# Performance work log

Measured on AMD Instinct MI355X. Metric: run time of the kernel, lower is better.

The kernel has to match this reference:

```python
import jax, jax.numpy as jnp
import numpy as np

NUM_HEADS = 16
LN_EPS = 1e-5


def pos_encoding(length, d):
    pos = jnp.arange(length, dtype=jnp.float32)[:, None]
    i = jnp.arange(d, dtype=jnp.float32)[None, :]
    angle = pos / jnp.power(10000.0, (2.0 * jnp.floor(i / 2.0)) / d)
    return jnp.where((jnp.arange(d) % 2) == 0, jnp.sin(angle), jnp.cos(angle))


def rel_shift(x):
    # x: (B, H, l, m) -> TXL shift trick
    b, h, l, m = x.shape
    x = jnp.concatenate([x, jnp.zeros((b, h, l, 1), x.dtype)], axis=-1)
    x = x.reshape(b, h, l * (m + 1))
    return x[:, :, l - 1:-1].reshape(b, h, l, m)


def layer_norm(x, g, b):
    mu = jnp.mean(x, axis=-1, keepdims=True)
    var = jnp.mean(jnp.square(x - mu), axis=-1, keepdims=True)
    return (x - mu) * jax.lax.rsqrt(var + LN_EPS) * g + b


def setup_inputs() -> dict:
    key = jax.random.key(0)
    B, S, M, D, L, V = 2, 1024, 1024, 1024, 4, 32000
    ks = jax.random.split(key, 32)
    s = 0.02
    d = {
        'inputs': jax.random.randint(ks[0], (B, S), 0, V, dtype=jnp.int32),
        'mems': jax.random.normal(ks[1], (L, B, M, D), jnp.float32),
        'emb': jax.random.normal(ks[2], (V, D), jnp.float32) * s,
        'Wq': jax.random.normal(ks[3], (L, D, D), jnp.float32) * s,
        'bq': jnp.zeros((L, D), jnp.float32),
        'Wke': jax.random.normal(ks[4], (L, D, D), jnp.float32) * s,
        'bke': jnp.zeros((L, D), jnp.float32),
        'Wkr': jax.random.normal(ks[5], (L, D, D), jnp.float32) * s,
        'bkr': jnp.zeros((L, D), jnp.float32),
        'Wv': jax.random.normal(ks[6], (L, D, D), jnp.float32) * s,
        'bv': jnp.zeros((L, D), jnp.float32),
        'Wo': jax.random.normal(ks[7], (L, D, D), jnp.float32) * s,
        'bo': jnp.zeros((L, D), jnp.float32),
        'ln1_g': jnp.ones((L, D), jnp.float32),
        'ln1_b': jnp.zeros((L, D), jnp.float32),
        'W1': jax.random.normal(ks[8], (L, D, D), jnp.float32) * s,
        'b1': jnp.zeros((L, D), jnp.float32),
        'W2': jax.random.normal(ks[9], (L, D, D), jnp.float32) * s,
        'b2': jnp.zeros((L, D), jnp.float32),
        'ln2_g': jnp.ones((L, D), jnp.float32),
        'ln2_b': jnp.zeros((L, D), jnp.float32),
        'Wh': jax.random.normal(ks[10], (D, D), jnp.float32) * s,
        'bh': jnp.zeros((D,), jnp.float32),
        'Wf': jax.random.normal(ks[11], (D, V), jnp.float32) * s,
        'bf': jnp.zeros((V,), jnp.float32),
        'next_mem_len': 1024,
    }
    return d


def reference(inputs, mems, emb, Wq, bq, Wke, bke, Wkr, bkr, Wv, bv, Wo, bo,
              ln1_g, ln1_b, W1, b1, W2, b2, ln2_g, ln2_b, Wh, bh, Wf, bf,
              next_mem_len):
    B, S = inputs.shape
    L, _, M, D = mems.shape
    T = M + S
    H = NUM_HEADS
    dh = D // H
    sqrt_dk = jnp.sqrt(jnp.float32(dh))

    rel_enc = pos_encoding(T, D)[::-1]  # (T, D), reversed
    # look-ahead mask: query i may attend key j iff j <= i + M
    mask = (jnp.arange(T)[None, :] > (jnp.arange(S)[:, None] + M)).astype(jnp.float32)
    mask = mask[None, None] * -1e9  # (1,1,S,T)

    x = emb[inputs] * jnp.sqrt(jnp.float32(D))  # (B,S,D)

    for l in range(L):
        x_tilde = jnp.concatenate([mems[l], x], axis=1)  # (B,T,D)
        q = (x @ Wq[l] + bq[l]).reshape(B, S, H, dh).transpose(0, 2, 1, 3)
        k = (x_tilde @ Wke[l] + bke[l]).reshape(B, T, H, dh).transpose(0, 2, 1, 3)
        v = (x_tilde @ Wv[l] + bv[l]).reshape(B, T, H, dh).transpose(0, 2, 1, 3)
        A = jnp.einsum('bhsd,bhtd->bhst', q, k)
        Qr = (rel_enc @ Wkr[l] + bkr[l]).reshape(T, H, dh).transpose(1, 0, 2)  # (H,T,dh)
        B_hat = jnp.einsum('bhsd,htd->bhst', q, Qr)
        score = (A + rel_shift(B_hat)) / sqrt_dk + mask
        attn = jax.nn.softmax(score, axis=-1)
        ctx = jnp.einsum('bhst,bhtd->bhsd', attn, v)
        ctx = ctx.transpose(0, 2, 1, 3).reshape(B, S, D)
        attn_out = ctx @ Wo[l] + bo[l]
        h1 = layer_norm(x + attn_out, ln1_g[l], ln1_b[l])
        ff = jax.nn.gelu(h1 @ W1[l] + b1[l], approximate=False) @ W2[l] + b2[l]
        x = layer_norm(h1 + ff, ln2_g[l], ln2_b[l])

    x = jax.nn.gelu(x @ Wh + bh, approximate=False)
    logits = x @ Wf + bf
    return logits
```

## Files before the change

### kernel.cpp

```cpp
#include <hip/hip_runtime.h>
#include <hip/hip_bf16.h>
#include <math.h>

typedef __attribute__((ext_vector_type(4))) float f32x4;
typedef __attribute__((ext_vector_type(8))) short s16x8;

#define BB 2
#define SS 1024
#define MEM 1024
#define DD 1024
#define LL 4
#define VV 32000
#define TT 2048
#define NH 16
#define DH 64

__device__ __forceinline__ short f2bf(float f) {
    unsigned u = __float_as_uint(f);
    u += 0x7fffu + ((u >> 16) & 1u);
    return (short)(u >> 16);
}

__device__ __forceinline__ float gelu_f(float x) {
    return 0.5f * x * (1.0f + erff(x * 0.70710678118654752f));
}

__device__ __forceinline__ void gll16(const short* g, short* l) {
    __builtin_amdgcn_global_load_lds(
        (__attribute__((address_space(1))) void*)(short*)g,
        (__attribute__((address_space(3))) void*)l, 16, 0, 0);
}

template<int N> __device__ __forceinline__ void vm_wait() {
    if constexpr (N == 0)      asm volatile("s_waitcnt vmcnt(0)" ::: "memory");
    else if constexpr (N == 2) asm volatile("s_waitcnt vmcnt(2)" ::: "memory");
    else if constexpr (N == 3) asm volatile("s_waitcnt vmcnt(3)" ::: "memory");
    else if constexpr (N == 4) asm volatile("s_waitcnt vmcnt(4)" ::: "memory");
    else if constexpr (N == 6) asm volatile("s_waitcnt vmcnt(6)" ::: "memory");
    else                       asm volatile("s_waitcnt vmcnt(8)" ::: "memory");
}

template<int WM, int WN>
__global__ __launch_bounds__(256) void gemm_bf16(
    const short* __restrict__ A, const short* __restrict__ Bt,
    const float* __restrict__ bias, const float* __restrict__ bias2,
    int nsplit, void* __restrict__ Cv, int N, int K, int nby, int act, int obf)
{
    constexpr int BM = WM * 32, BN = WN * 32;
    constexpr int NA = BM / 64, NB = BN / 64;
    constexpr int L  = NA + NB;
    constexpr int ASZ = BM * 32, BSZ = BN * 32;
    __shared__ short a_s[3 * ASZ];
    __shared__ short b_s[3 * BSZ];
    const int tid  = threadIdx.x;
    const int lane = tid & 63;
    const int wave = tid >> 6;
    const int wr = wave >> 1, wc = wave & 1;
    const int fr = lane & 15, fg = lane >> 4;

    const int nwg = gridDim.x;
    const int bid = blockIdx.x;
    const int swz = ((nwg & 7) == 0) ? ((bid & 7) * (nwg >> 3) + (bid >> 3)) : bid;
    const size_t m0 = (size_t)(swz % nby) * BM;
    const size_t n0 = (size_t)(swz / nby) * BN;

    const short* gA[NA]; short* lA[NA];
    const short* gB[NB]; short* lB[NB];
    #pragma unroll
    for (int i = 0; i < NA; ++i) {
        const int s   = i * 256 + tid;
        const int row = (s >> 6) * 16 + (s & 15);
        const int ks  = (s >> 4) & 3;
        gA[i] = A + (m0 + row) * (size_t)K + ks * 8;
        lA[i] = &a_s[s * 8];
    }
    #pragma unroll
    for (int i = 0; i < NB; ++i) {
        const int s   = i * 256 + tid;
        const int nn  = (s >> 6) * 16 + (s & 15);
        const int ks  = (s >> 4) & 3;
        gB[i] = Bt + (n0 + nn) * (size_t)K + ks * 8;
        lB[i] = &b_s[s * 8];
    }

    auto stage = [&](int t, int buf) {
        const int koff = t << 5;
        #pragma unroll
        for (int i = 0; i < NA; ++i) gll16(gA[i] + koff, lA[i] + buf * ASZ);
        #pragma unroll
        for (int i = 0; i < NB; ++i) gll16(gB[i] + koff, lB[i] + buf * BSZ);
    };

    f32x4 acc[WM][WN] = {};

    const int nt = K >> 5;
    stage(0, 0);
    stage(1, 1);

    int cur = 0;
    for (int t = 0; t < nt; ++t) {
        if (t + 1 < nt) vm_wait<L>();
        else            vm_wait<0>();
        __builtin_amdgcn_s_barrier();
        __builtin_amdgcn_sched_barrier(0);
        if (t + 2 < nt) stage(t + 2, cur == 0 ? 2 : cur - 1);

        const short* ab = &a_s[cur * ASZ];
        const short* bb = &b_s[cur * BSZ];
        s16x8 af[WM], bf[WN];
        #pragma unroll
        for (int mi = 0; mi < WM; ++mi)
            af[mi] = *(const s16x8*)&ab[((wr*WM + mi)*64 + fg*16 + fr) * 8];
        #pragma unroll
        for (int ni = 0; ni < WN; ++ni)
            bf[ni] = *(const s16x8*)&bb[((wc*WN + ni)*64 + fg*16 + fr) * 8];
        #pragma unroll
        for (int mi = 0; mi < WM; ++mi)
            #pragma unroll
            for (int ni = 0; ni < WN; ++ni)
                acc[mi][ni] = __builtin_amdgcn_mfma_f32_16x16x32_bf16(
                    af[mi], bf[ni], acc[mi][ni], 0, 0, 0);
        cur = (cur == 2) ? 0 : cur + 1;
    }

    float* Cf = (float*)Cv;
    short* Cb = (short*)Cv;
    #pragma unroll
    for (int mi = 0; mi < WM; ++mi) {
        #pragma unroll
        for (int ni = 0; ni < WN; ++ni) {
            const size_t r0 = m0 + wr*WM*16 + mi*16 + fg*4;
            const size_t c  = n0 + wc*WN*16 + ni*16 + fr;
            const float bb = (c < (size_t)nsplit) ? bias[c] : bias2[c - nsplit];
            #pragma unroll
            for (int rg = 0; rg < 4; ++rg) {
                float vv = acc[mi][ni][rg] + bb;
                if (act) vv = gelu_f(vv);
                if (obf) Cb[(r0 + rg)*(size_t)N + c] = f2bf(vv);
                else     Cf[(r0 + rg)*(size_t)N + c] = vv;
            }
        }
    }
}

__global__ __launch_bounds__(256) void transpose7_kernel(
    const float* w0, const float* w1, const float* w2, const float* w3,
    const float* w4, const float* w5, const float* w6, short* out)
{
    __shared__ float t[32][33];
    const int z = blockIdx.z;
    const float* W;
    switch (z) {
        case 0: W = w0; break; case 1: W = w1; break; case 2: W = w2; break;
        case 3: W = w3; break; case 4: W = w4; break; case 5: W = w5; break;
        default: W = w6; break;
    }
    short* O = out + (size_t)z * DD * DD;
    const int tid = threadIdx.x;
    const int k0 = blockIdx.y * 32, n0 = blockIdx.x * 32;
    const int r = tid >> 3, c4 = (tid & 7) * 4;
    float4 v = *(const float4*)&W[(size_t)(k0 + r) * DD + n0 + c4];
    t[r][c4+0] = v.x; t[r][c4+1] = v.y; t[r][c4+2] = v.z; t[r][c4+3] = v.w;
    __syncthreads();
    short4 o;
    o.x = f2bf(t[c4+0][r]); o.y = f2bf(t[c4+1][r]);
    o.z = f2bf(t[c4+2][r]); o.w = f2bf(t[c4+3][r]);
    *(short4*)&O[(size_t)(n0 + r) * DD + k0 + c4] = o;
}

__global__ __launch_bounds__(256) void transposeF_kernel(
    const float* __restrict__ W, short* __restrict__ O)
{
    __shared__ float t[32][33];
    const int tid = threadIdx.x;
    const int k0 = blockIdx.y * 32, n0 = blockIdx.x * 32;
    const int r = tid >> 3, c4 = (tid & 7) * 4;
    float4 v = *(const float4*)&W[(size_t)(k0 + r) * VV + n0 + c4];
    t[r][c4+0] = v.x; t[r][c4+1] = v.y; t[r][c4+2] = v.z; t[r][c4+3] = v.w;
    __syncthreads();
    short4 o;
    o.x = f2bf(t[c4+0][r]); o.y = f2bf(t[c4+1][r]);
    o.z = f2bf(t[c4+2][r]); o.w = f2bf(t[c4+3][r]);
    *(short4*)&O[(size_t)(n0 + r) * DD + k0 + c4] = o;
}

__global__ __launch_bounds__(256) void attn_kernel(
    const short* __restrict__ q, const short* __restrict__ k,
    const short* __restrict__ v, const short* __restrict__ Qr,
    short* __restrict__ ctx, int kstr, int qstr)
{
    __shared__ short k_s[64][72];
    __shared__ short vT_s[64][72];
    __shared__ short qr_s[128][72];
    __shared__ float a_t[64][67];
    __shared__ short p_s[64][72];

    const int tid  = threadIdx.x;
    const int id   = blockIdx.x;
    const int bh   = id & 31;
    const int qi   = ((id >> 5) + bh) & 15;
    const int q0   = qi * 64;
    const int b    = bh >> 4;
    const int h    = bh & 15;
    const int hoff = h * DH;

    const int lane = tid & 63;
    const int wave = tid >> 6;
    const int fr   = lane & 15;
    const int fg   = lane >> 4;
    const int tk = tid >> 2, ck = (tid & 3) * 16;
    const int rq = tid >> 1, dq = (tid & 1) * 32;
    const int sr  = tid >> 2;
    const int sc0 = (tid & 3) * 16;

    const short* qrow = q + ((size_t)(b * SS + q0 + 16 * wave + fr)) * DD + hoff;
    s16x8 aq0 = *(const s16x8*)(qrow + fg * 8);
    s16x8 aq1 = *(const s16x8*)(qrow + 32 + fg * 8);

    float m_r = -1e30f, l_r = 0.0f;

    const int t_end = q0 + 64 + MEM;
    const int u0b   = SS - 1 - q0 - 63;

    s16x8 kf0, kf1, vf0, vf1, rf0, rf1, rf2, rf3;
    auto loadT = [&](int t0) {
        const short* kp = k + ((size_t)(b * TT + t0 + tk)) * kstr + hoff + ck;
        const short* vp = v + ((size_t)(b * TT + t0 + tk)) * kstr + hoff + ck;
        kf0 = *(const s16x8*)kp;  kf1 = *(const s16x8*)(kp + 8);
        vf0 = *(const s16x8*)vp;  vf1 = *(const s16x8*)(vp + 8);
        int u = t0 + u0b + rq;
        u = u < 0 ? 0 : (u > TT - 1 ? TT - 1 : u);
        const short* rp = Qr + (size_t)u * qstr + hoff + dq;
        rf0 = *(const s16x8*)rp;        rf1 = *(const s16x8*)(rp + 8);
        rf2 = *(const s16x8*)(rp + 16); rf3 = *(const s16x8*)(rp + 24);
    };
    loadT(0);

    f32x4 opv[4] = {};
    const int nlo = 3 - wave, nhi = 7 - wave;

    for (int t0 = 0; t0 < t_end; t0 += 64) {
        asm volatile("" ::: "memory");
        __builtin_amdgcn_s_barrier();
        __builtin_amdgcn_sched_barrier(0);
        {
            *(s16x8*)&k_s[tk][ck]     = kf0;
            *(s16x8*)&k_s[tk][ck + 8] = kf1;
            #pragma unroll
            for (int i = 0; i < 8; ++i) {
                const int d0 = ck + i, d1 = ck + 8 + i;
                vT_s[d0][tk ^ (((d0 >> 3) & 3) << 3)] = vf0[i];
                vT_s[d1][tk ^ (((d1 >> 3) & 3) << 3)] = vf1[i];
            }
            *(s16x8*)&qr_s[rq][dq]      = rf0;
            *(s16x8*)&qr_s[rq][dq + 8]  = rf1;
            *(s16x8*)&qr_s[rq][dq + 16] = rf2;
            *(s16x8*)&qr_s[rq][dq + 24] = rf3;
        }
        if (t0 + 64 < t_end) loadT(t0 + 64);
        asm volatile("s_waitcnt lgkmcnt(0)" ::: "memory");
        __builtin_amdgcn_s_barrier();
        __builtin_amdgcn_sched_barrier(0);

        {
            #pragma unroll
            for (int n = 0; n < 4; ++n) {
                s16x8 b0 = *(const s16x8*)&k_s[16*n + fr][fg * 8];
                s16x8 b1 = *(const s16x8*)&k_s[16*n + fr][32 + fg * 8];
                f32x4 ca = {0, 0, 0, 0};
                ca = __builtin_amdgcn_mfma_f32_16x16x32_bf16(aq0, b0, ca, 0, 0, 0);
                ca = __builtin_amdgcn_mfma_f32_16x16x32_bf16(aq1, b1, ca, 0, 0, 0);
                #pragma unroll
                for (int rg = 0; rg < 4; ++rg)
                    a_t[16*wave + 4*fg + rg][16*n + fr] = ca[rg];
            }
        }
        {
            #pragma unroll
            for (int n = 0; n < 8; ++n) {
                if (n < nlo || n > nhi) continue;
                s16x8 c0 = *(const s16x8*)&qr_s[16*n + fr][fg * 8];
                s16x8 c1 = *(const s16x8*)&qr_s[16*n + fr][32 + fg * 8];
                f32x4 cb = {0, 0, 0, 0};
                cb = __builtin_amdgcn_mfma_f32_16x16x32_bf16(aq0, c0, cb, 0, 0, 0);
                cb = __builtin_amdgcn_mfma_f32_16x16x32_bf16(aq1, c1, cb, 0, 0, 0);
                #pragma unroll
                for (int rg = 0; rg < 4; ++rg) {
                    const int r  = 16*wave + 4*fg + rg;
                    const int tl = 16*n + fr - 63 + r;
                    if ((unsigned)tl < 64u) a_t[r][tl] += cb[rg];
                }
            }
        }

        {
            const int sg = q0 + sr;
            float e[16];
            float mx = -1e30f;
            #pragma unroll
            for (int j = 0; j < 16; ++j) {
                const int c = sc0 + j;
                float x = a_t[sr][c] * 0.125f;
                x = (t0 + c > sg + MEM) ? -1e30f : x;
                e[j] = x;
                mx = fmaxf(mx, x);
            }
            mx = fmaxf(mx, __shfl_xor(mx, 1, 64));
            mx = fmaxf(mx, __shfl_xor(mx, 2, 64));
            const float mn  = fmaxf(m_r, mx);
            const float scl = __expf(m_r - mn);
            float sum = 0.0f;
            s16x8 p0, p1;
            #pragma unroll
            for (int j = 0; j < 16; ++j) {
                float ev = __expf(e[j] - mn);
                sum += ev;
                if (j < 8) p0[j] = f2bf(ev); else p1[j - 8] = f2bf(ev);
            }
            sum += __shfl_xor(sum, 1, 64);
            sum += __shfl_xor(sum, 2, 64);
            l_r = l_r * scl + sum;
            m_r = mn;
            *(s16x8*)&p_s[sr][sc0]     = p0;
            *(s16x8*)&p_s[sr][sc0 + 8] = p1;

            f32x4 scv;
            #pragma unroll
            for (int rg = 0; rg < 4; ++rg) scv[rg] = __shfl(scl, 16*fg + 4*rg, 64);
            #pragma unroll
            for (int n = 0; n < 4; ++n)
                #pragma unroll
                for (int rg = 0; rg < 4; ++rg) opv[n][rg] *= scv[rg];
            s16x8 ap0 = *(const s16x8*)&p_s[16*wave + fr][fg * 8];
            s16x8 ap1 = *(const s16x8*)&p_s[16*wave + fr][32 + fg * 8];
            #pragma unroll
            for (int n = 0; n < 4; ++n) {
                const int d  = 16*n + fr;
                const int xw = (d >> 3) & 3;
                s16x8 bv0 = *(const s16x8*)&vT_s[d][(fg ^ xw) * 8];
                s16x8 bv1 = *(const s16x8*)&vT_s[d][32 + (fg ^ xw) * 8];
                opv[n] = __builtin_amdgcn_mfma_f32_16x16x32_bf16(ap0, bv0, opv[n], 0, 0, 0);
                opv[n] = __builtin_amdgcn_mfma_f32_16x16x32_bf16(ap1, bv1, opv[n], 0, 0, 0);
            }
        }
    }

    {
        f32x4 lv;
        #pragma unroll
        for (int rg = 0; rg < 4; ++rg) lv[rg] = __shfl(l_r, 16*fg + 4*rg, 64);
        #pragma unroll
        for (int rg = 0; rg < 4; ++rg) {
            const int r = 16*wave + 4*fg + rg;
            const float inv = 1.0f / lv[rg];
            short* op = ctx + ((size_t)(b * SS + q0 + r)) * DD + hoff;
            #pragma unroll
            for (int n = 0; n < 4; ++n)
                op[16*n + fr] = f2bf(opv[n][rg] * inv);
        }
    }
}

__global__ __launch_bounds__(256) void addln_kernel(
    const float* __restrict__ a, const float* __restrict__ b,
    const float* __restrict__ g, const float* __restrict__ be,
    float* __restrict__ out32, short* __restrict__ outbf)
{
    __shared__ float red[8];
    const int row = blockIdx.x;
    const int tid = threadIdx.x;
    const size_t base = (size_t)row * DD;
    const int c = tid * 4;
    float4 xa = *(const float4*)(a + base + c);
    float4 xb = *(const float4*)(b + base + c);
    float x0 = xa.x + xb.x, x1 = xa.y + xb.y, x2 = xa.z + xb.z, x3 = xa.w + xb.w;
    float s  = x0 + x1 + x2 + x3;
    float sq = x0 * x0 + x1 * x1 + x2 * x2 + x3 * x3;
    #pragma unroll
    for (int o = 32; o > 0; o >>= 1) {
        s  += __shfl_down(s, o, 64);
        sq += __shfl_down(sq, o, 64);
    }
    const int wv = tid >> 6;
    if ((tid & 63) == 0) { red[wv * 2] = s; red[wv * 2 + 1] = sq; }
    __syncthreads();
    float ts = red[0] + red[2] + red[4] + red[6];
    float tq = red[1] + red[3] + red[5] + red[7];
    float mu  = ts * (1.0f / DD);
    float var = tq * (1.0f / DD) - mu * mu;
    float rs  = rsqrtf(var + 1e-5f);
    float4 gv = *(const float4*)(g + c);
    float4 bv = *(const float4*)(be + c);
    float4 o4;
    o4.x = (x0 - mu) * rs * gv.x + bv.x;
    o4.y = (x1 - mu) * rs * gv.y + bv.y;
    o4.z = (x2 - mu) * rs * gv.z + bv.z;
    o4.w = (x3 - mu) * rs * gv.w + bv.w;
    *(float4*)(out32 + base + c) = o4;
    short4 ob;
    ob.x = f2bf(o4.x); ob.y = f2bf(o4.y); ob.z = f2bf(o4.z); ob.w = f2bf(o4.w);
    *(short4*)(outbf + base + c) = ob;
}

__global__ __launch_bounds__(256) void embed_kernel(
    const int* __restrict__ inp, const float* __restrict__ emb,
    float* __restrict__ x32, short* __restrict__ xbf)
{
    const int row = blockIdx.x;
    const int c = threadIdx.x * 4;
    const int idx = inp[row];
    float4 vv = *(const float4*)(emb + (size_t)idx * DD + c);
    vv.x *= 32.0f; vv.y *= 32.0f; vv.z *= 32.0f; vv.w *= 32.0f;
    *(float4*)(x32 + (size_t)row * DD + c) = vv;
    short4 ob;
    ob.x = f2bf(vv.x); ob.y = f2bf(vv.y); ob.z = f2bf(vv.z); ob.w = f2bf(vv.w);
    *(short4*)(xbf + (size_t)row * DD + c) = ob;
}

__global__ __launch_bounds__(256) void concat_kernel(
    const float* __restrict__ mems_l, const short* __restrict__ xbf,
    short* __restrict__ xt)
{
    size_t i = ((size_t)blockIdx.x * 256 + threadIdx.x) * 8;
    size_t bt = i / DD;
    int d = (int)(i - bt * DD);
    int b = (int)(bt / TT);
    int t = (int)(bt - (size_t)b * TT);
    s16x8 o;
    if (t < MEM) {
        const float* mp = mems_l + ((size_t)(b * MEM + t)) * DD + d;
        float4 a0 = *(const float4*)mp;
        float4 a1 = *(const float4*)(mp + 4);
        o[0] = f2bf(a0.x); o[1] = f2bf(a0.y); o[2] = f2bf(a0.z); o[3] = f2bf(a0.w);
        o[4] = f2bf(a1.x); o[5] = f2bf(a1.y); o[6] = f2bf(a1.z); o[7] = f2bf(a1.w);
    } else {
        o = *(const s16x8*)(xbf + ((size_t)(b * SS + (t - MEM))) * DD + d);
    }
    *(s16x8*)(xt + i) = o;
}

__global__ __launch_bounds__(256) void relenc_kernel(short* __restrict__ re)
{
    const int u = blockIdx.x;
    const int p = TT - 1 - u;
    const int i0 = threadIdx.x * 4;
    short4 o;
    #pragma unroll
    for (int j = 0; j < 4; ++j) {
        int i = i0 + j;
        float ex   = (float)(2 * (i >> 1)) * (1.0f / DD);
        float invf = __expf(-ex * 9.210340371976184f);
        float ang  = (float)p * invf;
        float val  = (i & 1) ? cosf(ang) : sinf(ang);
        ((short*)&o)[j] = f2bf(val);
    }
    *(short4*)&re[(size_t)u * DD + i0] = o;
}

extern "C" void kernel_launch(void* const* d_in, const int* in_sizes, int n_in,
                              void* d_out, int out_size, void* d_ws, size_t ws_size,
                              hipStream_t stream)
{
    const int*   inp  = (const int*)d_in[0];
    const float* mems = (const float*)d_in[1];
    const float* emb  = (const float*)d_in[2];
    const float* Wq   = (const float*)d_in[3];
    const float* bq   = (const float*)d_in[4];
    const float* Wke  = (const float*)d_in[5];
    const float* bke  = (const float*)d_in[6];
    const float* Wkr  = (const float*)d_in[7];
    const float* bkr  = (const float*)d_in[8];
    const float* Wv   = (const float*)d_in[9];
    const float* bv   = (const float*)d_in[10];
    const float* Wo   = (const float*)d_in[11];
    const float* bo   = (const float*)d_in[12];
    const float* ln1g = (const float*)d_in[13];
    const float* ln1b = (const float*)d_in[14];
    const float* W1   = (const float*)d_in[15];
    const float* b1   = (const float*)d_in[16];
    const float* W2   = (const float*)d_in[17];
    const float* b2   = (const float*)d_in[18];
    const float* ln2g = (const float*)d_in[19];
    const float* ln2b = (const float*)d_in[20];
    const float* Wh   = (const float*)d_in[21];
    const float* bh   = (const float*)d_in[22];
    const float* Wf   = (const float*)d_in[23];
    const float* bfb  = (const float*)d_in[24];

    char* wsb = (char*)d_ws;
    size_t off = 0;
    auto alloc = [&](size_t bytes) { char* p = wsb + off; off += (bytes + 255) & ~(size_t)255; return p; };
    float* h132  = (float*)alloc((size_t)BB*SS*DD*4);
    float* ao32  = (float*)alloc((size_t)BB*SS*DD*4);
    float* ff232 = (float*)alloc((size_t)BB*SS*DD*4);
    short* xt    = (short*)alloc((size_t)BB*TT*DD*2);
    short* qb    = (short*)alloc((size_t)BB*SS*DD*2);
    short* kvb   = (short*)alloc((size_t)BB*TT*DD*2*2);
    short* ctxb  = (short*)alloc((size_t)BB*SS*DD*2);
    short* ff1   = (short*)alloc((size_t)BB*SS*DD*2);
    float* x32   = (float*)alloc((size_t)BB*SS*DD*4);
    short* x_bf  = (short*)alloc((size_t)BB*SS*DD*2);
    short* whout = (short*)alloc((size_t)BB*SS*DD*2);
    short* rel   = (short*)alloc((size_t)TT*DD*2);
    short* qr4   = (short*)alloc((size_t)SS*2*4*DD*2);
    short* wt6   = (short*)alloc((size_t)6*DD*DD*2);
    short* wkr4  = (short*)h132;
    short* wft   = (short*)h132;

    relenc_kernel<<<TT, 256, 0, stream>>>(rel);
    embed_kernel<<<BB * SS, 256, 0, stream>>>(inp, emb, x32, x_bf);

    const size_t WOFF = (size_t)DD * DD;

    transpose7_kernel<<<dim3(32, 32, 4), 256, 0, stream>>>(
        Wkr + 0*WOFF, Wkr + 1*WOFF, Wkr + 2*WOFF, Wkr + 3*WOFF, Wq, Wq, Wq, wkr4);
    gemm_bf16<4,4><<<dim3(512), 256, 0, stream>>>(
        rel, wkr4, bkr, bkr, 4*DD, qr4, 4*DD, DD, TT/128, 0, 1);

    const int gSm = (DD / 64) * ((BB * SS) / 64);
    const int gKV = ((2 * DD) / 128) * ((BB * TT) / 128);

    for (int l = 0; l < LL; ++l) {
        const size_t wo  = (size_t)l * DD * DD;
        const size_t bo_ = (size_t)l * DD;
        transpose7_kernel<<<dim3(32, 32, 6), 256, 0, stream>>>(
            Wq + wo, Wke + wo, Wv + wo, Wo + wo, W1 + wo, W2 + wo, Wq, wt6);
        concat_kernel<<<(BB * TT * DD / 8) / 256, 256, 0, stream>>>(
            mems + (size_t)l * BB * MEM * DD, x_bf, xt);
        gemm_bf16<2,2><<<dim3(gSm), 256, 0, stream>>>(
            x_bf, wt6 + 0*WOFF, bq + bo_, bq + bo_, DD, qb, DD, DD, (BB*SS)/64, 0, 1);
        gemm_bf16<4,4><<<dim3(gKV), 256, 0, stream>>>(
            xt, wt6 + 1*WOFF, bke + bo_, bv + bo_, DD, kvb, 2*DD, DD, (BB*TT)/128, 0, 1);
        attn_kernel<<<dim3((SS / 64) * BB * NH), 256, 0, stream>>>(
            qb, kvb, kvb + DD, qr4 + (size_t)l * DD, ctxb, 2 * DD, 4 * DD);
        gemm_bf16<2,2><<<dim3(gSm), 256, 0, stream>>>(
            ctxb, wt6 + 3*WOFF, bo + bo_, bo + bo_, DD, ao32, DD, DD, (BB*SS)/64, 0, 0);
        addln_kernel<<<BB * SS, 256, 0, stream>>>(x32, ao32, ln1g + bo_, ln1b + bo_, h132, x_bf);
        gemm_bf16<2,2><<<dim3(gSm), 256, 0, stream>>>(
            x_bf, wt6 + 4*WOFF, b1 + bo_, b1 + bo_, DD, ff1, DD, DD, (BB*SS)/64, 1, 1);
        gemm_bf16<2,2><<<dim3(gSm), 256, 0, stream>>>(
            ff1, wt6 + 5*WOFF, b2 + bo_, b2 + bo_, DD, ff232, DD, DD, (BB*SS)/64, 0, 0);
        addln_kernel<<<BB * SS, 256, 0, stream>>>(h132, ff232, ln2g + bo_, ln2b + bo_, x32, x_bf);
    }

    transpose7_kernel<<<dim3(32, 32, 1), 256, 0, stream>>>(
        Wh, Wh, Wh, Wh, Wh, Wh, Wh, wt6);
    transposeF_kernel<<<dim3(VV / 32, DD / 32), 256, 0, stream>>>(Wf, wft);
    gemm_bf16<2,2><<<dim3(gSm), 256, 0, stream>>>(
        x_bf, wt6, bh, bh, DD, whout, DD, DD, (BB*SS)/64, 1, 1);
    gemm_bf16<4,4><<<dim3((VV / 128) * ((BB * SS) / 128)), 256, 0, stream>>>(
        whout, wft, bfb, bfb, VV, (float*)d_out, VV, DD, (BB*SS)/128, 0, 0);
}
```

Measured before the change: 1.451 ms.

## Add 256x256 8-wave ping-pong GEMM for vocab projection; simplify generic GEMM pipeline

Adds a new gemm8p kernel with 512 threads, 256x256 tiles, 128KB dynamic LDS double buffering, phased interleaving of loads and MFMAs with setprio and barriers, and uses it for the large final logits GEMM. The generic gemm_bf16 is also changed from a 3-stage 32-wide K pipeline to a single-buffer 64-wide K tile with two syncs per iteration. The aim is higher MFMA utilisation and more data reuse on the dominant vocab GEMM. The cost is that the generic GEMMs, used in every layer, lose their load/compute overlap. The new kernel hard-codes K=1024 and M=2048.

Result: faster. 1.271 ms (-12.4%).

```diff
diff --git a/kernel.cpp b/kernel.cpp
--- a/kernel.cpp
+++ b/kernel.cpp
@@ -31,15 +31,6 @@
         (__attribute__((address_space(3))) void*)l, 16, 0, 0);
 }
 
-template<int N> __device__ __forceinline__ void vm_wait() {
-    if constexpr (N == 0)      asm volatile("s_waitcnt vmcnt(0)" ::: "memory");
-    else if constexpr (N == 2) asm volatile("s_waitcnt vmcnt(2)" ::: "memory");
-    else if constexpr (N == 3) asm volatile("s_waitcnt vmcnt(3)" ::: "memory");
-    else if constexpr (N == 4) asm volatile("s_waitcnt vmcnt(4)" ::: "memory");
-    else if constexpr (N == 6) asm volatile("s_waitcnt vmcnt(6)" ::: "memory");
-    else                       asm volatile("s_waitcnt vmcnt(8)" ::: "memory");
-}
-
 template<int WM, int WN>
 __global__ __launch_bounds__(256) void gemm_bf16(
     const short* __restrict__ A, const short* __restrict__ Bt,
@@ -47,11 +38,9 @@
     int nsplit, void* __restrict__ Cv, int N, int K, int nby, int act, int obf)
 {
     constexpr int BM = WM * 32, BN = WN * 32;
-    constexpr int NA = BM / 64, NB = BN / 64;
-    constexpr int L  = NA + NB;
-    constexpr int ASZ = BM * 32, BSZ = BN * 32;
-    __shared__ short a_s[3 * ASZ];
-    __shared__ short b_s[3 * BSZ];
+    constexpr int NA = BM / 32, NB = BN / 32;
+    __shared__ short a_s[BM * 64];
+    __shared__ short b_s[BN * 64];
     const int tid  = threadIdx.x;
     const int lane = tid & 63;
     const int wave = tid >> 6;
@@ -69,58 +58,58 @@
     #pragma unroll
     for (int i = 0; i < NA; ++i) {
         const int s   = i * 256 + tid;
-        const int row = (s >> 6) * 16 + (s & 15);
-        const int ks  = (s >> 4) & 3;
-        gA[i] = A + (m0 + row) * (size_t)K + ks * 8;
+        const int row = (s >> 7) * 16 + (s & 15);
+        const int kof = ((s >> 4) & 7) * 8;
+        gA[i] = A + (m0 + row) * (size_t)K + kof;
         lA[i] = &a_s[s * 8];
     }
     #pragma unroll
     for (int i = 0; i < NB; ++i) {
         const int s   = i * 256 + tid;
-        const int nn  = (s >> 6) * 16 + (s & 15);
-        const int ks  = (s >> 4) & 3;
-        gB[i] = Bt + (n0 + nn) * (size_t)K + ks * 8;
+        const int nn  = (s >> 7) * 16 + (s & 15);
+        const int kof = ((s >> 4) & 7) * 8;
+        gB[i] = Bt + (n0 + nn) * (size_t)K + kof;
         lB[i] = &b_s[s * 8];
     }
 
-    auto stage = [&](int t, int buf) {
-        const int koff = t << 5;
-        #pragma unroll
-        for (int i = 0; i < NA; ++i) gll16(gA[i] + koff, lA[i] + buf * ASZ);
-        #pragma unroll
-        for (int i = 0; i < NB; ++i) gll16(gB[i] + koff, lB[i] + buf * BSZ);
-    };
-
     f32x4 acc[WM][WN] = {};
 
-    const int nt = K >> 5;
-    stage(0, 0);
-    stage(1, 1);
-
-    int cur = 0;
+    #pragma unroll
+    for (int i = 0; i < NA; ++i) gll16(gA[i], lA[i]);
+    #pragma unroll
+    for (int i = 0; i < NB; ++i) gll16(gB[i], lB[i]);
+
+    const int nt = K >> 6;
     for (int t = 0; t < nt; ++t) {
-        if (t + 1 < nt) vm_wait<L>();
-        else            vm_wait<0>();
-        __builtin_amdgcn_s_barrier();
-        __builtin_amdgcn_sched_barrier(0);
-        if (t + 2 < nt) stage(t + 2, cur == 0 ? 2 : cur - 1);
-
-        const short* ab = &a_s[cur * ASZ];
-        const short* bb = &b_s[cur * BSZ];
-        s16x8 af[WM], bf[WN];
+        __syncthreads();
+        s16x8 af[WM][2], bf[WN][2];
         #pragma unroll
         for (int mi = 0; mi < WM; ++mi)
-            af[mi] = *(const s16x8*)&ab[((wr*WM + mi)*64 + fg*16 + fr) * 8];
+            #pragma unroll
+            for (int h = 0; h < 2; ++h)
+                af[mi][h] = *(const s16x8*)&a_s[((wr*WM + mi)*128 + (h*4 + fg)*16 + fr) * 8];
         #pragma unroll
         for (int ni = 0; ni < WN; ++ni)
-            bf[ni] = *(const s16x8*)&bb[((wc*WN + ni)*64 + fg*16 + fr) * 8];
+            #pragma unroll
+            for (int h = 0; h < 2; ++h)
+                bf[ni][h] = *(const s16x8*)&b_s[((wc*WN + ni)*128 + (h*4 + fg)*16 + fr) * 8];
+        if (t + 1 < nt) {
+            __syncthreads();
+            const int koff = (t + 1) << 6;
+            #pragma unroll
+            for (int i = 0; i < NA; ++i) gll16(gA[i] + koff, lA[i]);
+            #pragma unroll
+            for (int i = 0; i < NB; ++i) gll16(gB[i] + koff, lB[i]);
+        }
         #pragma unroll
         for (int mi = 0; mi < WM; ++mi)
             #pragma unroll
-            for (int ni = 0; ni < WN; ++ni)
+            for (int ni = 0; ni < WN; ++ni) {
                 acc[mi][ni] = __builtin_amdgcn_mfma_f32_16x16x32_bf16(
-                    af[mi], bf[ni], acc[mi][ni], 0, 0, 0);
-        cur = (cur == 2) ? 0 : cur + 1;
+                    af[mi][0], bf[ni][0], acc[mi][ni], 0, 0, 0);
+                acc[mi][ni] = __builtin_amdgcn_mfma_f32_16x16x32_bf16(
+                    af[mi][1], bf[ni][1], acc[mi][ni], 0, 0, 0);
+            }
     }
 
     float* Cf = (float*)Cv;
@@ -139,6 +128,109 @@
                 if (obf) Cb[(r0 + rg)*(size_t)N + c] = f2bf(vv);
                 else     Cf[(r0 + rg)*(size_t)N + c] = vv;
             }
+        }
+    }
+}
+
+#define READ_A8(MH, BUF) \
+  _Pragma("unroll") for (int mf = 0; mf < 4; ++mf) \
+  _Pragma("unroll") for (int kh = 0; kh < 2; ++kh) \
+    aA[mf][kh] = *(const s16x8*)&lds[(BUF)*16384 + WR*8192 + (((MH)*4+mf)*128 + (kh*4+fg)*16 + fr)*8];
+
+#define READ_B8(BUF) \
+  _Pragma("unroll") for (int nf = 0; nf < 4; ++nf) \
+  _Pragma("unroll") for (int kh = 0; kh < 2; ++kh) \
+    bB[nf][kh] = *(const s16x8*)&lds[32768 + (BUF)*16384 + BH*8192 + ((BC4+nf)*128 + (kh*4+fg)*16 + fr)*8];
+
+#define QUAD8(MH, NH) \
+  _Pragma("unroll") for (int mf = 0; mf < 4; ++mf) \
+  _Pragma("unroll") for (int n2 = 0; n2 < 2; ++n2) { \
+    acc[(MH)*4+mf][(NH)*2+n2] = __builtin_amdgcn_mfma_f32_16x16x32_bf16( \
+        aA[mf][0], bB[(NH)*2+n2][0], acc[(MH)*4+mf][(NH)*2+n2], 0, 0, 0); \
+    acc[(MH)*4+mf][(NH)*2+n2] = __builtin_amdgcn_mfma_f32_16x16x32_bf16( \
+        aA[mf][1], bB[(NH)*2+n2][1], acc[(MH)*4+mf][(NH)*2+n2], 0, 0, 0); }
+
+#define STAGE_A8(HH, BUF, KT) { \
+    const short* g = pA0 + (HH)*(128*1024) + (KT)*64; \
+    short* l = &lds[(BUF)*16384 + (HH)*8192 + tid*8]; \
+    gll16(g, l); gll16(g + 64*1024, l + 512*8); }
+
+#define STAGE_B8(HH, BUF, KT) { \
+    const short* g = pB0 + (HH)*(128*1024) + (KT)*64; \
+    short* l = &lds[32768 + (BUF)*16384 + (HH)*8192 + tid*8]; \
+    gll16(g, l); gll16(g + 64*1024, l + 512*8); }
+
+#define PHASE8(BUF, MH, NH, RA, RB, SMAT, SH, SBUF, SKT, VMW) { \
+    if (RA) { READ_A8(MH, BUF) } \
+    if (RB) { READ_B8(BUF) } \
+    if ((SMAT) == 0) STAGE_A8(SH, SBUF, SKT) else STAGE_B8(SH, SBUF, SKT) \
+    __builtin_amdgcn_s_barrier(); \
+    asm volatile("s_waitcnt lgkmcnt(0)" ::: "memory"); \
+    __builtin_amdgcn_sched_barrier(0); \
+    __builtin_amdgcn_s_setprio(1); \
+    QUAD8(MH, NH) \
+    __builtin_amdgcn_s_setprio(0); \
+    if (VMW) { asm volatile("s_waitcnt vmcnt(4)" ::: "memory"); } \
+    __builtin_amdgcn_s_barrier(); }
+
+__global__ __launch_bounds__(512, 2) void gemm8p(
+    const short* __restrict__ A, const short* __restrict__ Bt,
+    const float* __restrict__ bias, float* __restrict__ C, int N)
+{
+    extern __shared__ short lds[];
+    const int tid  = threadIdx.x;
+    const int lane = tid & 63;
+    const int wave = tid >> 6;
+    const int WR = wave >> 2;
+    const int WC = wave & 3;
+    const int BH = WC >> 1;
+    const int BC4 = (WC & 1) * 4;
+    const int fr = lane & 15, fg = lane >> 4;
+
+    const int nwg = gridDim.x;
+    const int bid = blockIdx.x;
+    const int swz = ((nwg & 7) == 0) ? ((bid & 7) * (nwg >> 3) + (bid >> 3)) : bid;
+    const size_t m0 = (size_t)(swz % 8) * 256;
+    const size_t n0 = (size_t)(swz / 8) * 256;
+
+    const int arow0 = (tid >> 7) * 16 + (tid & 15);
+    const int aks0  = ((tid >> 4) & 7) * 8;
+    const short* pA0 = A  + (m0 + arow0) * 1024 + aks0;
+    const short* pB0 = Bt + (n0 + arow0) * 1024 + aks0;
+
+    f32x4 acc[8][4] = {};
+    s16x8 aA[4][2], bB[4][2];
+
+    STAGE_B8(0, 0, 0) STAGE_B8(1, 0, 0)
+    STAGE_A8(0, 0, 0) STAGE_A8(1, 0, 0)
+    STAGE_B8(0, 1, 1) STAGE_B8(1, 1, 1)
+    asm volatile("s_waitcnt vmcnt(4)" ::: "memory");
+    __builtin_amdgcn_s_barrier();
+
+    for (int it = 0; it < 8; ++it) {
+        const int k1 = 2*it + 1;
+        int k2 = 2*it + 2; if (k2 > 15) k2 = 15;
+        int k3 = 2*it + 3; if (k3 > 15) k3 = 15;
+        PHASE8(0, 0, 0, 1, 1, 0, 0, 1, k1, 0)
+        PHASE8(0, 0, 1, 0, 0, 0, 1, 1, k1, 0)
+        PHASE8(0, 1, 0, 1, 0, 1, 0, 0, k2, 0)
+        PHASE8(0, 1, 1, 0, 0, 1, 1, 0, k2, 1)
+        PHASE8(1, 0, 0, 1, 1, 0, 0, 0, k2, 0)
+        PHASE8(1, 0, 1, 0, 0, 0, 1, 0, k2, 0)
+        PHASE8(1, 1, 0, 1, 0, 1, 0, 1, k3, 0)
+        PHASE8(1, 1, 1, 0, 0, 1, 1, 1, k3, 1)
+    }
+
+    #pragma unroll
+    for (int mf = 0; mf < 8; ++mf) {
+        #pragma unroll
+        for (int nf = 0; nf < 4; ++nf) {
+            const size_t r0 = m0 + WR*128 + mf*16 + fg*4;
+            const size_t c  = n0 + WC*64 + nf*16 + fr;
+            const float bb = bias[c];
+            #pragma unroll
+            for (int rg = 0; rg < 4; ++rg)
+                C[(r0 + rg) * (size_t)N + c] = acc[mf][nf][rg] + bb;
         }
     }
 }
@@ -487,6 +579,9 @@
     const float* Wf   = (const float*)d_in[23];
     const float* bfb  = (const float*)d_in[24];
 
+    hipFuncSetAttribute((const void*)gemm8p,
+                        hipFuncAttributeMaxDynamicSharedMemorySize, 131072);
+
     char* wsb = (char*)d_ws;
     size_t off = 0;
     auto alloc = [&](size_t bytes) { char* p = wsb + off; off += (bytes + 255) & ~(size_t)255; return p; };
@@ -548,6 +643,6 @@
     transposeF_kernel<<<dim3(VV / 32, DD / 32), 256, 0, stream>>>(Wf, wft);
     gemm_bf16<2,2><<<dim3(gSm), 256, 0, stream>>>(
         x_bf, wt6, bh, bh, DD, whout, DD, DD, (BB*SS)/64, 1, 1);
-    gemm_bf16<4,4><<<dim3((VV / 128) * ((BB * SS) / 128)), 256, 0, stream>>>(
-        whout, wft, bfb, bfb, VV, (float*)d_out, VV, DD, (BB*SS)/128, 0, 0);
-}
+    gemm8p<<<dim3((VV / 256) * ((BB * SS) / 256)), 512, 131072, stream>>>(
+        whout, wft, bfb, (float*)d_out, VV);
+}
```
